# Kernel tuning notes

Measured on AMD Instinct MI355X. Metric: run time of the kernel, lower is better.

## Reference

```python
import jax, jax.numpy as jnp
import numpy as np


def setup_inputs() -> dict:
    key = jax.random.key(0)
    ks = jax.random.split(key, 10)
    B, S, I, H = 32, 512, 256, 512
    stdv = 1.0 / np.sqrt(H)
    u = lambda k, shape: jax.random.uniform(k, shape, jnp.float32, -stdv, stdv)
    return {
        "inputs": jax.random.normal(ks[0], (B, S, I), jnp.float32),
        "h0": jax.random.normal(ks[1], (2, B, H), jnp.float32),
        "weight_ih_f": u(ks[2], (H, I)),
        "weight_hh_f": u(ks[3], (H, H)),
        "bias_ih_f": u(ks[4], (H,)),
        "bias_hh_f": u(ks[5], (H,)),
        "weight_ih_b": u(ks[6], (H, I)),
        "weight_hh_b": u(ks[7], (H, H)),
        "bias_ih_b": u(ks[8], (H,)),
        "bias_hh_b": u(ks[9], (H,)),
    }


def _rnn_direction(x_proj, h0, weight_hh):
    # x_proj: [S, B, H] precomputed input projection + biases; h0: [B, H]
    def step(h, xp):
        h_new = jax.nn.relu(xp + h @ weight_hh.T)
        return h_new, h_new
    hn, outs = jax.lax.scan(step, h0, x_proj)
    return hn, outs  # outs: [S, B, H]


def reference(inputs, h0, weight_ih_f, weight_hh_f, bias_ih_f, bias_hh_f,
              weight_ih_b, weight_hh_b, bias_ih_b, bias_hh_b):
    # inputs: [B, S, I]; h0: [2, B, H]
    x_sbI = jnp.swapaxes(inputs, 0, 1)  # [S, B, I]
    # Hoist the input GEMM out of the recurrence (math identical).
    xp_f = x_sbI @ weight_ih_f.T + bias_ih_f + bias_hh_f  # [S, B, H]
    xp_b = x_sbI @ weight_ih_b.T + bias_ih_b + bias_hh_b
    hn_f, outs_f = _rnn_direction(xp_f, h0[0], weight_hh_f)
    # backward direction: scan reversed sequence, then flip outputs back
    hn_b, outs_b_rev = _rnn_direction(xp_b[::-1], h0[1], weight_hh_b)
    outs_b = outs_b_rev[::-1]
    outputs = jnp.concatenate((outs_f, outs_b), axis=-1)  # [S, B, 2H]
    outputs = jnp.swapaxes(outputs, 0, 1)  # [B, S, 2H]
    hn = jnp.stack((hn_f, hn_b), axis=0)  # [2, B, H]
    return outputs, hn
```

## Files before the change

### kernel.cpp

```cpp
#include <hip/hip_runtime.h>
#include <stdint.h>

#define B_ 32
#define S_ 512
#define I_ 256
#define H_ 512
#define OUTW 1024
#define OUTS_ELEMS (B_*S_*OUTW)

typedef _Float16 f16;
typedef _Float16 half2_t __attribute__((ext_vector_type(2)));

__device__ __forceinline__ float fdot2(uint32_t a, uint32_t b, float c){
#if __has_builtin(__builtin_amdgcn_fdot2)
  return __builtin_amdgcn_fdot2(__builtin_bit_cast(half2_t, a),
                                __builtin_bit_cast(half2_t, b), c, false);
#else
  half2_t ha = __builtin_bit_cast(half2_t, a);
  half2_t hb = __builtin_bit_cast(half2_t, b);
  return c + (float)ha.x*(float)hb.x + (float)ha.y*(float)hb.y;
#endif
}

__device__ __forceinline__ uint32_t packf16(float x, float y){
  union { f16 h[2]; uint32_t u; } z;
  z.h[0] = (f16)x; z.h[1] = (f16)y;
  return z.u;
}

template<int CTRL>
__device__ __forceinline__ float dpp_xor_add(float x){
  int v = __builtin_amdgcn_update_dpp(0, __float_as_int(x), CTRL, 0xF, 0xF, true);
  return x + __int_as_float(v);
}

__device__ __forceinline__ int swz16(int chunk){
  return (chunk & ~7) | ((chunk ^ (chunk >> 3)) & 7);
}

__global__ __launch_bounds__(256) void cvt_w_kernel(const float* __restrict__ wf,
                                                    const float* __restrict__ wb,
                                                    f16* __restrict__ out){
  int i = blockIdx.x*256 + threadIdx.x;
  const float* src = (i < 32768) ? wf : wb;
  int base = (i & 32767) * 8;
  float4 a = *(const float4*)(src + base);
  float4 c = *(const float4*)(src + base + 4);
  uint4 o;
  o.x = packf16(a.x, a.y); o.y = packf16(a.z, a.w);
  o.z = packf16(c.x, c.y); o.w = packf16(c.z, c.w);
  *(uint4*)(out + (size_t)i*8) = o;
}

#define PTM 128
#define PTN 64
#define PTK 32
__global__ __launch_bounds__(256) void proj_kernel(
    const float* __restrict__ x,
    const float* __restrict__ wihf, const float* __restrict__ wihb,
    const float* __restrict__ bihf, const float* __restrict__ bhhf,
    const float* __restrict__ bihb, const float* __restrict__ bhhb,
    float* __restrict__ out)
{
  __shared__ float As[PTK][132];
  __shared__ float Bs[PTK][68];
  const int tid = threadIdx.x;
  const int row0 = blockIdx.x * PTM;
  const int j0   = blockIdx.y * PTN;
  const int dir  = (j0 >= 512) ? 1 : 0;
  const int jl0  = j0 - dir*512;
  const float* wih = dir ? wihb : wihf;
  const float* bi  = dir ? bihb : bihf;
  const float* bh  = dir ? bhhb : bhhf;

  const int ty = tid >> 4, tx = tid & 15;
  float acc[8][4];
#pragma unroll
  for (int i=0;i<8;i++)
#pragma unroll
    for (int j=0;j<4;j++) acc[i][j] = 0.f;

  float bias[4];
#pragma unroll
  for (int jj=0;jj<4;jj++){ int jl = jl0 + tx*4 + jj; bias[jj] = bi[jl] + bh[jl]; }

  for (int k0 = 0; k0 < I_; k0 += PTK){
    {
      int r = tid >> 1, kh = (tid & 1) * 16;
      int rg = row0 + r; int bb = rg & 31, tt = rg >> 5;
      const float* ap = x + ((size_t)bb*S_ + tt)*I_ + k0 + kh;
#pragma unroll
      for (int u=0;u<4;u++){
        float4 v = *(const float4*)(ap + u*4);
        As[kh+u*4+0][r] = v.x; As[kh+u*4+1][r] = v.y;
        As[kh+u*4+2][r] = v.z; As[kh+u*4+3][r] = v.w;
      }
    }
    {
      int jr = tid >> 2, kh = (tid & 3) * 8;
      const float* bp = wih + (size_t)(jl0 + jr)*I_ + k0 + kh;
#pragma unroll
      for (int u=0;u<2;u++){
        float4 v = *(const float4*)(bp + u*4);
        Bs[kh+u*4+0][jr] = v.x; Bs[kh+u*4+1][jr] = v.y;
        Bs[kh+u*4+2][jr] = v.z; Bs[kh+u*4+3][jr] = v.w;
      }
    }
    __syncthreads();
#pragma unroll 8
    for (int kk=0; kk<PTK; ++kk){
      const float4 a0 = *(const float4*)&As[kk][ty*8+0];
      const float4 a1 = *(const float4*)&As[kk][ty*8+4];
      const float4 bq = *(const float4*)&Bs[kk][tx*4];
      const float av[8] = {a0.x,a0.y,a0.z,a0.w,a1.x,a1.y,a1.z,a1.w};
      const float bv[4] = {bq.x,bq.y,bq.z,bq.w};
#pragma unroll
      for (int i=0;i<8;i++)
#pragma unroll
        for (int j=0;j<4;j++) acc[i][j] = fmaf(av[i], bv[j], acc[i][j]);
    }
    __syncthreads();
  }
#pragma unroll
  for (int i=0;i<8;i++){
    int rg = row0 + ty*8 + i; int bb = rg & 31, tt = rg >> 5;
    float* op = out + ((size_t)bb*S_ + tt)*OUTW + j0 + tx*4;
    float4 v = {acc[i][0]+bias[0], acc[i][1]+bias[1], acc[i][2]+bias[2], acc[i][3]+bias[3]};
    *(float4*)op = v;
  }
}

#define MAIL_OFF_U32 (1u<<18)

__global__ __launch_bounds__(512, 2) void rnn_kernel(
    const f16* __restrict__ Wall,
    const float* __restrict__ h0,
    float* dout, uint32_t* mailbase)
{
  __shared__ char lds[2048];
  const int tid  = threadIdx.x;
  const int g    = blockIdx.x;
  const int dir  = g >> 6;
  const int b    = (g >> 1) & 31;
  const int half = g & 1;
  const int jg   = tid >> 3;
  const int ks   = tid & 7;
  const int k3   = ks & 3;
  const bool owner = (ks < 4);
  const int jl   = jg + 64*k3;

  const f16* Wd = Wall + (size_t)dir * (H_*(size_t)H_);
  float* outs = dout + (size_t)b * (S_*OUTW);
  const int col = dir*512 + half*256 + jl;
  float* hn = dout + (size_t)OUTS_ELEMS + ((size_t)dir*B_ + b) * H_;

  uint32_t* mail = mailbase;
  const int pairid = dir*32 + b;
  uint32_t* mw = mail + ((size_t)pairid*2 + half) * 512;
  uint32_t* mr = mail + ((size_t)pairid*2 + (half^1)) * 512;

  uint32_t wL[4][16], wR[4][16];
#pragma unroll
  for (int r=0;r<4;r++){
    const f16* row = Wd + (size_t)(half*256 + jg + 64*r) * H_;
    const uint4* pL = (const uint4*)(row + half*256 + ks*32);
    const uint4* pR = (const uint4*)(row + (half^1)*256 + ks*32);
#pragma unroll
    for (int q=0;q<4;q++){
      uint4 v = pL[q];
      wL[r][q*4+0]=v.x; wL[r][q*4+1]=v.y; wL[r][q*4+2]=v.z; wL[r][q*4+3]=v.w;
      uint4 u = pR[q];
      wR[r][q*4+0]=u.x; wR[r][q*4+1]=u.y; wR[r][q*4+2]=u.z; wR[r][q*4+3]=u.w;
    }
  }

  int oL[4], oR[4];
#pragma unroll
  for (int q=0;q<4;q++){
    oL[q] = swz16(half*32     + ks*4 + q) * 16;
    oR[q] = swz16((half^1)*32 + ks*4 + q) * 16;
  }
  const int kO = half*256 + jl;
  const int oO = swz16(kO>>3)*16 + (kO&7)*2;
  const int kS = (half^1)*256 + tid;
  const int oS = swz16(kS>>3)*16 + (kS&7)*2;

  {
    int k = tid;
    int off = swz16(k>>3)*16 + (k&7)*2;
    *(f16*)(lds + 1024 + off) = (f16)h0[((size_t)dir*B_ + b)*H_ + k];
  }
  __syncthreads();

  for (int s=0; s<S_; ++s){
    const int t = dir ? (S_-1-s) : s;
    const int P = (s+1)&1;
    char* hb = lds + P*1024;
    float* xo = outs + (size_t)t*OUTW;
    float xpv = 0.f;
    if (owner) xpv = xo[col];

    float a0=0.f, a1=0.f, a2=0.f, a3=0.f;
#pragma unroll
    for (int q=0;q<4;q++){
      const uint4 hv = *(const uint4*)(hb + oL[q]);
      a0 = fdot2(wL[0][q*4+0],hv.x,a0); a0 = fdot2(wL[0][q*4+1],hv.y,a0);
      a0 = fdot2(wL[0][q*4+2],hv.z,a0); a0 = fdot2(wL[0][q*4+3],hv.w,a0);
      a1 = fdot2(wL[1][q*4+0],hv.x,a1); a1 = fdot2(wL[1][q*4+1],hv.y,a1);
      a1 = fdot2(wL[1][q*4+2],hv.z,a1); a1 = fdot2(wL[1][q*4+3],hv.w,a1);
      a2 = fdot2(wL[2][q*4+0],hv.x,a2); a2 = fdot2(wL[2][q*4+1],hv.y,a2);
      a2 = fdot2(wL[2][q*4+2],hv.z,a2); a2 = fdot2(wL[2][q*4+3],hv.w,a2);
      a3 = fdot2(wL[3][q*4+0],hv.x,a3); a3 = fdot2(wL[3][q*4+1],hv.y,a3);
      a3 = fdot2(wL[3][q*4+2],hv.z,a3); a3 = fdot2(wL[3][q*4+3],hv.w,a3);
    }
    if (s > 0 && tid < 256){
      const uint32_t tag = (uint32_t)s & 0xffffu;
      uint32_t v;
      do {
        v = __hip_atomic_load(&mr[P*256 + tid], __ATOMIC_RELAXED, __HIP_MEMORY_SCOPE_AGENT);
      } while ((v & 0xffffu) != tag);
      uint16_t hb16 = (uint16_t)(v >> 16);
      *(f16*)(hb + oS) = __builtin_bit_cast(f16, hb16);
    }
    __syncthreads();
#pragma unroll
    for (int q=0;q<4;q++){
      const uint4 hv = *(const uint4*)(hb + oR[q]);
      a0 = fdot2(wR[0][q*4+0],hv.x,a0); a0 = fdot2(wR[0][q*4+1],hv.y,a0);
      a0 = fdot2(wR[0][q*4+2],hv.z,a0); a0 = fdot2(wR[0][q*4+3],hv.w,a0);
      a1 = fdot2(wR[1][q*4+0],hv.x,a1); a1 = fdot2(wR[1][q*4+1],hv.y,a1);
      a1 = fdot2(wR[1][q*4+2],hv.z,a1); a1 = fdot2(wR[1][q*4+3],hv.w,a1);
      a2 = fdot2(wR[2][q*4+0],hv.x,a2); a2 = fdot2(wR[2][q*4+1],hv.y,a2);
      a2 = fdot2(wR[2][q*4+2],hv.z,a2); a2 = fdot2(wR[2][q*4+3],hv.w,a2);
      a3 = fdot2(wR[3][q*4+0],hv.x,a3); a3 = fdot2(wR[3][q*4+1],hv.y,a3);
      a3 = fdot2(wR[3][q*4+2],hv.z,a3); a3 = fdot2(wR[3][q*4+3],hv.w,a3);
    }
    a0 = dpp_xor_add<0xB1>(a0); a1 = dpp_xor_add<0xB1>(a1);
    a2 = dpp_xor_add<0xB1>(a2); a3 = dpp_xor_add<0xB1>(a3);
    a0 = dpp_xor_add<0x4E>(a0); a1 = dpp_xor_add<0x4E>(a1);
    a2 = dpp_xor_add<0x4E>(a2); a3 = dpp_xor_add<0x4E>(a3);
    float own = (k3==0)?a0:(k3==1)?a1:(k3==2)?a2:a3;
    float tot = own + __shfl_xor(own, 4);

    if (owner){
      float h = fmaxf(xpv + tot, 0.f);
      xo[col] = h;
      if (s == S_-1) hn[half*256 + jl] = h;
      uint16_t hb16 = __builtin_bit_cast(uint16_t, (f16)h);
      *(f16*)(lds + (P^1)*1024 + oO) = __builtin_bit_cast(f16, hb16);
      uint32_t val = ((uint32_t)hb16 << 16) | ((uint32_t)(s+1) & 0xffffu);
      __hip_atomic_store(&mw[(P^1)*256 + jl], val, __ATOMIC_RELAXED, __HIP_MEMORY_SCOPE_AGENT);
    }
    __syncthreads();
  }
}

extern "C" void kernel_launch(void* const* d_in, const int* in_sizes, int n_in,
                              void* d_out, int out_size, void* d_ws, size_t ws_size,
                              hipStream_t stream){
  const float* x    = (const float*)d_in[0];
  const float* h0   = (const float*)d_in[1];
  const float* wihf = (const float*)d_in[2];
  const float* whhf = (const float*)d_in[3];
  const float* bihf = (const float*)d_in[4];
  const float* bhhf = (const float*)d_in[5];
  const float* wihb = (const float*)d_in[6];
  const float* whhb = (const float*)d_in[7];
  const float* bihb = (const float*)d_in[8];
  const float* bhhb = (const float*)d_in[9];
  float* out = (float*)d_out;
  f16* wf16 = (f16*)d_ws;
  uint32_t* mail = (uint32_t*)d_ws + MAIL_OFF_U32;

  cvt_w_kernel<<<256, 256, 0, stream>>>(whhf, whhb, wf16);
  proj_kernel<<<dim3(128, 16), 256, 0, stream>>>(x, wihf, wihb, bihf, bhhf, bihb, bhhb, out);
  rnn_kernel<<<128, 512, 0, stream>>>(wf16, h0, out, mail);
}
```

Before: 660.7 us.

## Exchange partial sums instead of hidden state between paired RNN blocks

```diff
diff --git a/kernel.cpp b/kernel.cpp
--- a/kernel.cpp
+++ b/kernel.cpp
@@ -34,8 +34,13 @@
   return x + __int_as_float(v);
 }
 
-__device__ __forceinline__ int swz16(int chunk){
-  return (chunk & ~7) | ((chunk ^ (chunk >> 3)) & 7);
+__device__ __forceinline__ float reduce8(float a0, float a1, float a2, float a3, int k3){
+  a0 = dpp_xor_add<0xB1>(a0); a1 = dpp_xor_add<0xB1>(a1);
+  a2 = dpp_xor_add<0xB1>(a2); a3 = dpp_xor_add<0xB1>(a3);
+  a0 = dpp_xor_add<0x4E>(a0); a1 = dpp_xor_add<0x4E>(a1);
+  a2 = dpp_xor_add<0x4E>(a2); a3 = dpp_xor_add<0x4E>(a3);
+  float own = (k3==0)?a0:(k3==1)?a1:(k3==2)?a2:a3;
+  return own + __shfl_xor(own, 4);
 }
 
 __global__ __launch_bounds__(256) void cvt_w_kernel(const float* __restrict__ wf,
@@ -131,127 +136,114 @@
 }
 
 #define MAIL_OFF_U32 (1u<<18)
+#define MAIL_BYTES   (64*2*2*256*4)
+
+#define PIN16(A) asm volatile("" : \
+  "+v"(A[0]),"+v"(A[1]),"+v"(A[2]),"+v"(A[3]),"+v"(A[4]),"+v"(A[5]),"+v"(A[6]),"+v"(A[7]), \
+  "+v"(A[8]),"+v"(A[9]),"+v"(A[10]),"+v"(A[11]),"+v"(A[12]),"+v"(A[13]),"+v"(A[14]),"+v"(A[15]))
+
+#define DOT4(ACC, WM, HV, Q) \
+  ACC = fdot2(WM[Q*4+0], HV.x, ACC); ACC = fdot2(WM[Q*4+1], HV.y, ACC); \
+  ACC = fdot2(WM[Q*4+2], HV.z, ACC); ACC = fdot2(WM[Q*4+3], HV.w, ACC);
+
+#define PHASE16(W, A0,A1,A2,A3) \
+  DOT4(A0, W[0], hv0, 0) DOT4(A0, W[0], hv1, 1) DOT4(A0, W[0], hv2, 2) DOT4(A0, W[0], hv3, 3) \
+  DOT4(A1, W[1], hv0, 0) DOT4(A1, W[1], hv1, 1) DOT4(A1, W[1], hv2, 2) DOT4(A1, W[1], hv3, 3) \
+  DOT4(A2, W[2], hv0, 0) DOT4(A2, W[2], hv1, 1) DOT4(A2, W[2], hv2, 2) DOT4(A2, W[2], hv3, 3) \
+  DOT4(A3, W[3], hv0, 0) DOT4(A3, W[3], hv1, 1) DOT4(A3, W[3], hv2, 2) DOT4(A3, W[3], hv3, 3)
 
 __global__ __launch_bounds__(512, 2) void rnn_kernel(
     const f16* __restrict__ Wall,
     const float* __restrict__ h0,
     float* dout, uint32_t* mailbase)
 {
-  __shared__ char lds[2048];
-  const int tid  = threadIdx.x;
-  const int g    = blockIdx.x;
-  const int dir  = g >> 6;
-  const int b    = (g >> 1) & 31;
-  const int half = g & 1;
-  const int jg   = tid >> 3;
-  const int ks   = tid & 7;
-  const int k3   = ks & 3;
-  const bool owner = (ks < 4);
-  const int jl   = jg + 64*k3;
+  __shared__ char lds[1024];
+  const int tid   = threadIdx.x;
+  const int half  = blockIdx.x >> 6;
+  const int pairid= blockIdx.x & 63;
+  const int dir   = pairid >> 5;
+  const int b     = pairid & 31;
+  const int jg    = tid >> 3;
+  const int ks    = tid & 7;
+  const int k3    = ks & 3;
+  const bool owner= (ks < 4);
+  const int jl    = jg + 64*k3;
 
   const f16* Wd = Wall + (size_t)dir * (H_*(size_t)H_);
   float* outs = dout + (size_t)b * (S_*OUTW);
   const int col = dir*512 + half*256 + jl;
   float* hn = dout + (size_t)OUTS_ELEMS + ((size_t)dir*B_ + b) * H_;
 
-  uint32_t* mail = mailbase;
-  const int pairid = dir*32 + b;
-  uint32_t* mw = mail + ((size_t)pairid*2 + half) * 512;
-  uint32_t* mr = mail + ((size_t)pairid*2 + (half^1)) * 512;
-
-  uint32_t wL[4][16], wR[4][16];
-#pragma unroll
-  for (int r=0;r<4;r++){
-    const f16* row = Wd + (size_t)(half*256 + jg + 64*r) * H_;
-    const uint4* pL = (const uint4*)(row + half*256 + ks*32);
-    const uint4* pR = (const uint4*)(row + (half^1)*256 + ks*32);
+  uint32_t* mw = mailbase + ((size_t)pairid*2 + half) * 512;
+  uint32_t* mr = mailbase + ((size_t)pairid*2 + (half^1)) * 512;
+
+  uint32_t wA[4][16], wB[4][16];
+#pragma unroll
+  for (int m=0;m<4;m++){
+    const uint4* pA = (const uint4*)(Wd + (size_t)((half^1)*256 + jg + 64*m)*H_ + half*256 + ks*32);
+    const uint4* pB = (const uint4*)(Wd + (size_t)( half*256     + jg + 64*m)*H_ + half*256 + ks*32);
 #pragma unroll
     for (int q=0;q<4;q++){
-      uint4 v = pL[q];
-      wL[r][q*4+0]=v.x; wL[r][q*4+1]=v.y; wL[r][q*4+2]=v.z; wL[r][q*4+3]=v.w;
-      uint4 u = pR[q];
-      wR[r][q*4+0]=u.x; wR[r][q*4+1]=u.y; wR[r][q*4+2]=u.z; wR[r][q*4+3]=u.w;
-    }
-  }
-
-  int oL[4], oR[4];
-#pragma unroll
-  for (int q=0;q<4;q++){
-    oL[q] = swz16(half*32     + ks*4 + q) * 16;
-    oR[q] = swz16((half^1)*32 + ks*4 + q) * 16;
-  }
-  const int kO = half*256 + jl;
-  const int oO = swz16(kO>>3)*16 + (kO&7)*2;
-  const int kS = (half^1)*256 + tid;
-  const int oS = swz16(kS>>3)*16 + (kS&7)*2;
-
-  {
-    int k = tid;
-    int off = swz16(k>>3)*16 + (k&7)*2;
-    *(f16*)(lds + 1024 + off) = (f16)h0[((size_t)dir*B_ + b)*H_ + k];
+      uint4 v = pA[q];
+      wA[m][q*4+0]=v.x; wA[m][q*4+1]=v.y; wA[m][q*4+2]=v.z; wA[m][q*4+3]=v.w;
+      uint4 u = pB[q];
+      wB[m][q*4+0]=u.x; wB[m][q*4+1]=u.y; wB[m][q*4+2]=u.z; wB[m][q*4+3]=u.w;
+    }
+  }
+
+  const int hwoff = (((jl>>3)&3)*8 + (jl>>5))*16 + (jl&7)*2;
+  if (tid < 256){
+    int off = (((tid>>3)&3)*8 + (tid>>5))*16 + (tid&7)*2;
+    *(f16*)(lds + off) = (f16)h0[((size_t)dir*B_ + b)*H_ + half*256 + tid];
   }
   __syncthreads();
 
   for (int s=0; s<S_; ++s){
+    PIN16(wA[0]); PIN16(wA[1]); PIN16(wA[2]); PIN16(wA[3]);
+    PIN16(wB[0]); PIN16(wB[1]); PIN16(wB[2]); PIN16(wB[3]);
+
+    const int P = s & 1;
     const int t = dir ? (S_-1-s) : s;
-    const int P = (s+1)&1;
-    char* hb = lds + P*1024;
+    const char* hb = lds + P*512;
     float* xo = outs + (size_t)t*OUTW;
     float xpv = 0.f;
     if (owner) xpv = xo[col];
 
-    float a0=0.f, a1=0.f, a2=0.f, a3=0.f;
-#pragma unroll
-    for (int q=0;q<4;q++){
-      const uint4 hv = *(const uint4*)(hb + oL[q]);
-      a0 = fdot2(wL[0][q*4+0],hv.x,a0); a0 = fdot2(wL[0][q*4+1],hv.y,a0);
-      a0 = fdot2(wL[0][q*4+2],hv.z,a0); a0 = fdot2(wL[0][q*4+3],hv.w,a0);
-      a1 = fdot2(wL[1][q*4+0],hv.x,a1); a1 = fdot2(wL[1][q*4+1],hv.y,a1);
-      a1 = fdot2(wL[1][q*4+2],hv.z,a1); a1 = fdot2(wL[1][q*4+3],hv.w,a1);
-      a2 = fdot2(wL[2][q*4+0],hv.x,a2); a2 = fdot2(wL[2][q*4+1],hv.y,a2);
-      a2 = fdot2(wL[2][q*4+2],hv.z,a2); a2 = fdot2(wL[2][q*4+3],hv.w,a2);
-      a3 = fdot2(wL[3][q*4+0],hv.x,a3); a3 = fdot2(wL[3][q*4+1],hv.y,a3);
-      a3 = fdot2(wL[3][q*4+2],hv.z,a3); a3 = fdot2(wL[3][q*4+3],hv.w,a3);
-    }
-    if (s > 0 && tid < 256){
-      const uint32_t tag = (uint32_t)s & 0xffffu;
+    const uint4 hv0 = *(const uint4*)(hb +       ks*16);
+    const uint4 hv1 = *(const uint4*)(hb + 128 + ks*16);
+    const uint4 hv2 = *(const uint4*)(hb + 256 + ks*16);
+    const uint4 hv3 = *(const uint4*)(hb + 384 + ks*16);
+
+    {
+      float a0=0.f, a1=0.f, a2=0.f, a3=0.f;
+      PHASE16(wA, a0,a1,a2,a3)
+      float totA = reduce8(a0,a1,a2,a3,k3);
+      if (owner){
+        uint16_t pb = __builtin_bit_cast(uint16_t, (f16)totA);
+        uint32_t val = ((uint32_t)pb << 16) | (uint32_t)(s+1);
+        __hip_atomic_store(&mw[P*256 + jl], val, __ATOMIC_RELAXED, __HIP_MEMORY_SCOPE_AGENT);
+      }
+    }
+    float totB;
+    {
+      float b0=0.f, b1=0.f, b2=0.f, b3=0.f;
+      PHASE16(wB, b0,b1,b2,b3)
+      totB = reduce8(b0,b1,b2,b3,k3);
+    }
+    if (owner){
+      const uint32_t tag = (uint32_t)(s+1);
       uint32_t v;
       do {
-        v = __hip_atomic_load(&mr[P*256 + tid], __ATOMIC_RELAXED, __HIP_MEMORY_SCOPE_AGENT);
+        v = __hip_atomic_load(&mr[P*256 + jl], __ATOMIC_RELAXED, __HIP_MEMORY_SCOPE_AGENT);
       } while ((v & 0xffffu) != tag);
-      uint16_t hb16 = (uint16_t)(v >> 16);
-      *(f16*)(hb + oS) = __builtin_bit_cast(f16, hb16);
-    }
-    __syncthreads();
-#pragma unroll
-    for (int q=0;q<4;q++){
-      const uint4 hv = *(const uint4*)(hb + oR[q]);
-      a0 = fdot2(wR[0][q*4+0],hv.x,a0); a0 = fdot2(wR[0][q*4+1],hv.y,a0);
-      a0 = fdot2(wR[0][q*4+2],hv.z,a0); a0 = fdot2(wR[0][q*4+3],hv.w,a0);
-      a1 = fdot2(wR[1][q*4+0],hv.x,a1); a1 = fdot2(wR[1][q*4+1],hv.y,a1);
-      a1 = fdot2(wR[1][q*4+2],hv.z,a1); a1 = fdot2(wR[1][q*4+3],hv.w,a1);
-      a2 = fdot2(wR[2][q*4+0],hv.x,a2); a2 = fdot2(wR[2][q*4+1],hv.y,a2);
-      a2 = fdot2(wR[2][q*4+2],hv.z,a2); a2 = fdot2(wR[2][q*4+3],hv.w,a2);
-      a3 = fdot2(wR[3][q*4+0],hv.x,a3); a3 = fdot2(wR[3][q*4+1],hv.y,a3);
-      a3 = fdot2(wR[3][q*4+2],hv.z,a3); a3 = fdot2(wR[3][q*4+3],hv.w,a3);
-    }
-    a0 = dpp_xor_add<0xB1>(a0); a1 = dpp_xor_add<0xB1>(a1);
-    a2 = dpp_xor_add<0xB1>(a2); a3 = dpp_xor_add<0xB1>(a3);
-    a0 = dpp_xor_add<0x4E>(a0); a1 = dpp_xor_add<0x4E>(a1);
-    a2 = dpp_xor_add<0x4E>(a2); a3 = dpp_xor_add<0x4E>(a3);
-    float own = (k3==0)?a0:(k3==1)?a1:(k3==2)?a2:a3;
-    float tot = own + __shfl_xor(own, 4);
-
-    if (owner){
-      float h = fmaxf(xpv + tot, 0.f);
+      float rem = (float)__builtin_bit_cast(f16, (uint16_t)(v >> 16));
+      float h = fmaxf(xpv + totB + rem, 0.f);
       xo[col] = h;
       if (s == S_-1) hn[half*256 + jl] = h;
-      uint16_t hb16 = __builtin_bit_cast(uint16_t, (f16)h);
-      *(f16*)(lds + (P^1)*1024 + oO) = __builtin_bit_cast(f16, hb16);
-      uint32_t val = ((uint32_t)hb16 << 16) | ((uint32_t)(s+1) & 0xffffu);
-      __hip_atomic_store(&mw[(P^1)*256 + jl], val, __ATOMIC_RELAXED, __HIP_MEMORY_SCOPE_AGENT);
-    }
-    __syncthreads();
+      *(f16*)(lds + (P^1)*512 + hwoff) = (f16)h;
+    }
+    asm volatile("s_waitcnt lgkmcnt(0)" ::: "memory");
+    __builtin_amdgcn_s_barrier();
   }
 }
 
@@ -272,6 +264,7 @@
   f16* wf16 = (f16*)d_ws;
   uint32_t* mail = (uint32_t*)d_ws + MAIL_OFF_U32;
 
+  hipMemsetAsync((void*)mail, 0, MAIL_BYTES, stream);
   cvt_w_kernel<<<256, 256, 0, stream>>>(whhf, whhb, wf16);
   proj_kernel<<<dim3(128, 16), 256, 0, stream>>>(x, wihf, wihb, bihf, bhhf, bihb, bhhb, out);
   rnn_kernel<<<128, 512, 0, stream>>>(wf16, h0, out, mail);
```

Measured after the change: 1.013 ms. +53.3%, slower.
